# Optimization experiments

Measured on AMD Instinct MI355X. Metric: run time of the kernel, lower is better.

## Reference

```python
import jax, jax.numpy as jnp
import numpy as np

D_MODEL = 1024
N_HEADS = 16
HEAD_DIM = D_MODEL // N_HEADS
B, T = 2, 2048

def setup_inputs() -> dict:
    key = jax.random.key(0)
    ks = jax.random.split(key, 9)
    s = 1.0 / np.sqrt(D_MODEL)
    return {
        "x": jax.random.normal(ks[0], (B, T, D_MODEL), dtype=jnp.float32),
        "Wq": jax.random.normal(ks[1], (D_MODEL, D_MODEL), dtype=jnp.float32) * s,
        "bq": jax.random.normal(ks[2], (D_MODEL,), dtype=jnp.float32) * 0.01,
        "Wk": jax.random.normal(ks[3], (D_MODEL, D_MODEL), dtype=jnp.float32) * s,
        "bk": jax.random.normal(ks[4], (D_MODEL,), dtype=jnp.float32) * 0.01,
        "Wv": jax.random.normal(ks[5], (D_MODEL, D_MODEL), dtype=jnp.float32) * s,
        "bv": jax.random.normal(ks[6], (D_MODEL,), dtype=jnp.float32) * 0.01,
        "Wo": jax.random.normal(ks[7], (D_MODEL, D_MODEL), dtype=jnp.float32) * s,
        "bo": jax.random.normal(ks[8], (D_MODEL,), dtype=jnp.float32) * 0.01,
    }

def reference(x, Wq, bq, Wk, bk, Wv, bv, Wo, bo):
    b, t, c = x.shape
    # Projections; reshape to [B, H, T, Dh]
    def heads(w, bias):
        return (x @ w.T + bias).reshape(b, t, N_HEADS, HEAD_DIM).transpose(0, 2, 1, 3)
    q = heads(Wq, bq)
    k = heads(Wk, bk)
    v = heads(Wv, bv)
    scale = 1.0 / np.sqrt(HEAD_DIM)
    att = jnp.einsum("bhqd,bhkd->bhqk", q, k) * scale  # [B,H,T,T]
    causal = jnp.tril(jnp.ones((t, t), dtype=bool))
    att = jnp.where(causal, att, -jnp.inf)
    att = jax.nn.softmax(att, axis=-1)
    # dropout p=0.0 (eval) -> identity
    y = jnp.einsum("bhqk,bhkd->bhqd", att, v)  # [B,H,T,Dh]
    y = y.transpose(0, 2, 1, 3).reshape(b, t, c)
    return y @ Wo.T + bo
```

## Files before the change

### kernel.cpp

```cpp
#include <hip/hip_runtime.h>
#include <stdint.h>


typedef unsigned short u16;
typedef __attribute__((ext_vector_type(8)))  __bf16 bf16x8;
typedef __attribute__((ext_vector_type(4)))  float  f32x4;
typedef __attribute__((ext_vector_type(16))) float  f32x16;
typedef __attribute__((ext_vector_type(4)))  float  float4v;
typedef __attribute__((ext_vector_type(4)))  unsigned short u16x4;
typedef __attribute__((ext_vector_type(4)))  unsigned int   u32x4;
typedef __attribute__((ext_vector_type(8)))  short  short8;

#define BB 2
#define TT 2048
#define DD 1024
#define HH 16
#define DH 64
#define MM (BB*TT)
#define NSLOT 2304
#define CEXP 0.18033688011f

static __device__ __forceinline__ u16 f2bf(float f) {
    uint32_t u = __builtin_bit_cast(uint32_t, f);
    u += 0x7FFFu + ((u >> 16) & 1u);
    return (u16)(u >> 16);
}
static __device__ __forceinline__ float bf2f(u16 v) {
    uint32_t u = (uint32_t)v << 16;
    return __builtin_bit_cast(float, u);
}

static __device__ __forceinline__ unsigned cvt_pk_bf16(float a, float b) {
    unsigned r;
    asm("v_cvt_pk_bf16_f32 %0, %1, %2" : "=v"(r) : "v"(a), "v"(b));
    return r;
}

static __device__ __forceinline__ void load_lds16(const u16* g, const u16* lds_base) {
    __builtin_amdgcn_global_load_lds(
        (const __attribute__((address_space(1))) void*)(uintptr_t)g,
        (__attribute__((address_space(3)))  void*)(uint32_t)(uintptr_t)lds_base,
        16u, 0, 0u);
}

static __device__ __forceinline__ f32x4 mfma16(bf16x8 a, bf16x8 b, f32x4 c) {
    return __builtin_amdgcn_mfma_f32_16x16x32_bf16(a, b, c, 0, 0, 0);
}
static __device__ __forceinline__ f32x16 mfma32(bf16x8 a, bf16x8 b, f32x16 c) {
    return __builtin_amdgcn_mfma_f32_32x32x16_bf16(a, b, c, 0, 0, 0);
}

static __device__ __forceinline__ float tree_sum16(const f32x16& a) {
    float m[8];
#pragma unroll
    for (int r = 0; r < 8; ++r) m[r] = a[r] + a[r + 8];
#pragma unroll
    for (int off = 4; off; off >>= 1)
#pragma unroll
        for (int r = 0; r < off; ++r) m[r] += m[r + off];
    return m[0];
}

static __device__ __forceinline__ bf16x8 pack8(float s0, float s1, float s2,
        float s3, float s4, float s5, float s6, float s7) {
    unsigned c0 = cvt_pk_bf16(s0, s1);
    unsigned c1 = cvt_pk_bf16(s2, s3);
    unsigned c2 = cvt_pk_bf16(s4, s5);
    unsigned c3 = cvt_pk_bf16(s6, s7);
    asm volatile("v_permlane32_swap_b32 %0, %1" : "+v"(c0), "+v"(c2));
    asm volatile("v_permlane32_swap_b32 %0, %1" : "+v"(c1), "+v"(c3));
    u32x4 w; w[0] = c0; w[1] = c1; w[2] = c2; w[3] = c3;
    return __builtin_bit_cast(bf16x8, w);
}

__global__ __launch_bounds__(256) void cvt_kernel(const float* __restrict__ src,
                                                  u16* __restrict__ dst, int n4) {
    int i = blockIdx.x * blockDim.x + threadIdx.x;
    int stride = gridDim.x * blockDim.x;
    for (; i < n4; i += stride) {
        float4v v = ((const float4v*)src)[i];
        u16x4 o;
        o[0] = f2bf(v[0]); o[1] = f2bf(v[1]); o[2] = f2bf(v[2]); o[3] = f2bf(v[3]);
        ((u16x4*)dst)[i] = o;
    }
}

__global__ __launch_bounds__(256) void cvt4_kernel(const float* __restrict__ s0,
        const float* __restrict__ s1, const float* __restrict__ s2,
        const float* __restrict__ s3, u16* __restrict__ d0, u16* __restrict__ d1,
        u16* __restrict__ d2, u16* __restrict__ d3, int n4) {
    const int z = blockIdx.y;
    const float* src = (z == 0) ? s0 : (z == 1) ? s1 : (z == 2) ? s2 : s3;
    u16* dst = (z == 0) ? d0 : (z == 1) ? d1 : (z == 2) ? d2 : d3;
    const float sc = (z == 0) ? CEXP : 1.0f;
    int i = blockIdx.x * blockDim.x + threadIdx.x;
    int stride = gridDim.x * blockDim.x;
    for (; i < n4; i += stride) {
        float4v v = ((const float4v*)src)[i];
        u16x4 o;
        o[0] = f2bf(v[0] * sc); o[1] = f2bf(v[1] * sc);
        o[2] = f2bf(v[2] * sc); o[3] = f2bf(v[3] * sc);
        ((u16x4*)dst)[i] = o;
    }
}

template<int OUTF32>
__global__ __launch_bounds__(256) void gemm_nt(const u16* __restrict__ A,
        const u16* __restrict__ W,
        const float* __restrict__ b0, const float* __restrict__ b1,
        const float* __restrict__ b2, float qsc,
        u16* __restrict__ outb, float* __restrict__ outf,
        int M, int N, int K) {
    __shared__ alignas(16) u16 As[128 * 32];
    __shared__ alignas(16) u16 Bs[128 * 32];

    const int tid  = threadIdx.x;
    const int wave = tid >> 6, lane = tid & 63;
    const int lr = lane & 15, lg = lane >> 4;
    const int wr = wave >> 1, wc = wave & 1;
    const int z  = blockIdx.z;
    const int m0 = blockIdx.x * 128;
    const int n0 = blockIdx.y * 128;

    const u16* Wz = W + (size_t)z * N * K;
    const float* bias = (z == 0) ? b0 : (z == 1) ? b1 : b2;
    const float bsc = (z == 0) ? qsc : 1.0f;

    f32x4 acc[4][4];
#pragma unroll
    for (int m = 0; m < 4; ++m)
#pragma unroll
        for (int n = 0; n < 4; ++n) acc[m][n] = (f32x4){0.f, 0.f, 0.f, 0.f};

    for (int k0 = 0; k0 < K; k0 += 32) {
        __syncthreads();
#pragma unroll
        for (int it = 0; it < 2; ++it) {
            int c = it * 256 + tid;
            int row = c >> 2, cc = (c & 3) * 8;
            const u16* gA = A  + (size_t)(m0 + row) * K + k0 + cc;
            const u16* gB = Wz + (size_t)(n0 + row) * K + k0 + cc;
            load_lds16(gA, As + (size_t)(it * 256 + wave * 64) * 8);
            load_lds16(gB, Bs + (size_t)(it * 256 + wave * 64) * 8);
        }
        __syncthreads();

        bf16x8 af[4], bfm[4];
#pragma unroll
        for (int m = 0; m < 4; ++m)
            af[m] = *(const bf16x8*)&As[(wr * 64 + m * 16 + lr) * 32 + lg * 8];
#pragma unroll
        for (int n = 0; n < 4; ++n)
            bfm[n] = *(const bf16x8*)&Bs[(wc * 64 + n * 16 + lr) * 32 + lg * 8];
#pragma unroll
        for (int m = 0; m < 4; ++m)
#pragma unroll
            for (int n = 0; n < 4; ++n)
                acc[m][n] = mfma16(af[m], bfm[n], acc[m][n]);
    }

#pragma unroll
    for (int n = 0; n < 4; ++n) {
        int col = n0 + wc * 64 + n * 16 + lr;
        float bv = bias[col] * bsc;
#pragma unroll
        for (int m = 0; m < 4; ++m) {
            int row = m0 + wr * 64 + m * 16 + lg * 4;
            if (OUTF32 == 0 && z == 2) {
                u16* vt = outb + (size_t)2 * M * N;
                size_t base = ((size_t)(((row >> 11) * 16 + (col >> 6)) * 64
                                        + (col & 63))) * 2048 + (row & 2047);
                u16x4 pv;
#pragma unroll
                for (int r = 0; r < 4; ++r) pv[r] = f2bf(acc[m][n][r] + bv);
                *(u16x4*)&vt[base] = pv;
            } else {
#pragma unroll
                for (int r = 0; r < 4; ++r) {
                    float v = acc[m][n][r] + bv;
                    if (OUTF32 == 0)
                        outb[(size_t)z * M * N + (size_t)(row + r) * N + col] = f2bf(v);
                    else
                        outf[(size_t)(row + r) * N + col] = v;
                }
            }
        }
    }
}

__global__ __launch_bounds__(256) void attn_part(const u16* __restrict__ Qb,
        const u16* __restrict__ Kb, const u16* __restrict__ VTb,
        u16* __restrict__ Op, float* __restrict__ Ml, u16* __restrict__ Yb) {
    __shared__ alignas(16) u16 Ks[64 * 64];
    __shared__ alignas(16) u16 Vs[64 * 64];

    const int tid  = threadIdx.x;
    const int wave = tid >> 6, lane = tid & 63;
    const int lq = lane & 31, hi = lane >> 5;

    const int i0 = blockIdx.x;
    const int bh = (i0 & 7) * 4 + ((i0 >> 3) / 72);
    const int s  = (i0 >> 3) % 72;
    int qi = 0, ch = 0;
    {
        int cum = 0, found = 0;
#pragma unroll
        for (int j = 0; j < 16; ++j) {
            int n = (j + 2) >> 1;
            if (!found && s < cum + n) { qi = j; ch = s - cum; found = 1; }
            cum += n;
        }
    }
    const int nc = (qi + 2) >> 1;
    const int b = bh >> 4, h = bh & 15;
    const size_t rb = (size_t)b * TT;
    const int hoff = h * DH;
    const int q0w = qi * 128 + wave * 32;
    const int k0 = ch * 256;
    const int kend = qi * 128 + 128;
    const int k1 = (k0 + 256 < kend) ? k0 + 256 : kend;

    const int srow0 = tid >> 3, sl = tid & 7;
    const int srow1 = (256 + tid) >> 3;

    const u16* Kbh = Kb + rb * DD + hoff;
    const u16* Vbh = VTb + (size_t)bh * 64 * 2048;

    bf16x8 qf[4];
    {
        const u16* qrow = Qb + (rb + q0w + lq) * DD + hoff + hi * 8;
#pragma unroll
        for (int kc = 0; kc < 4; ++kc) qf[kc] = *(const bf16x8*)(qrow + kc * 16);
    }

    f32x16 o0 = {}, o1 = {};
    float l_i = 0.f;

    for (int kv0 = k0; kv0 < k1; kv0 += 64) {
        __syncthreads();
        load_lds16(Kbh + (size_t)(kv0 + srow0) * DD + (sl ^ (srow0 & 7)) * 8,
                   &Ks[(size_t)(wave * 64) * 8]);
        load_lds16(Kbh + (size_t)(kv0 + srow1) * DD + (sl ^ (srow1 & 7)) * 8,
                   &Ks[(size_t)(256 + wave * 64) * 8]);
        load_lds16(Vbh + (size_t)srow0 * 2048 + kv0 + (sl ^ (srow0 & 7)) * 8,
                   &Vs[(size_t)(wave * 64) * 8]);
        load_lds16(Vbh + (size_t)srow1 * 2048 + kv0 + (sl ^ (srow1 & 7)) * 8,
                   &Vs[(size_t)(256 + wave * 64) * 8]);
        __syncthreads();

        if (kv0 < q0w + 32) {
            const int rowm = lq & 7;
            const bool diag = (kv0 + 63 > q0w);
            const int qrel = q0w + lq - kv0;
            bf16x8 pb[4];

            {
                f32x16 st = {};
#pragma unroll
                for (int kc = 0; kc < 4; ++kc) {
                    bf16x8 kf = *(const bf16x8*)&Ks[lq * 64 + ((2 * kc + hi) ^ rowm) * 8];
                    st = mfma32(kf, qf[kc], st);
                }
                if (diag) {
#pragma unroll
                    for (int r = 0; r < 16; ++r) {
                        int key = (r & 3) + 8 * (r >> 2) + 4 * hi;
                        if (key > qrel) st[r] = -1e30f;
                    }
                }
#pragma unroll
                for (int r = 0; r < 16; ++r) st[r] = __builtin_amdgcn_exp2f(st[r]);
                l_i += tree_sum16(st);
                pb[0] = pack8(st[0], st[1], st[2], st[3], st[4], st[5], st[6], st[7]);
                pb[1] = pack8(st[8], st[9], st[10], st[11], st[12], st[13], st[14], st[15]);
            }
            {
                f32x16 st = {};
#pragma unroll
                for (int kc = 0; kc < 4; ++kc) {
                    bf16x8 kf = *(const bf16x8*)&Ks[(32 + lq) * 64 + ((2 * kc + hi) ^ rowm) * 8];
                    st = mfma32(kf, qf[kc], st);
                }
                if (diag) {
#pragma unroll
                    for (int r = 0; r < 16; ++r) {
                        int key = 32 + (r & 3) + 8 * (r >> 2) + 4 * hi;
                        if (key > qrel) st[r] = -1e30f;
                    }
                }
#pragma unroll
                for (int r = 0; r < 16; ++r) st[r] = __builtin_amdgcn_exp2f(st[r]);
                l_i += tree_sum16(st);
                pb[2] = pack8(st[0], st[1], st[2], st[3], st[4], st[5], st[6], st[7]);
                pb[3] = pack8(st[8], st[9], st[10], st[11], st[12], st[13], st[14], st[15]);
            }

#pragma unroll
            for (int ks = 0; ks < 4; ++ks) {
                bf16x8 vf0 = *(const bf16x8*)&Vs[lq * 64        + ((ks * 2 + hi) ^ rowm) * 8];
                bf16x8 vf1 = *(const bf16x8*)&Vs[(32 + lq) * 64 + ((ks * 2 + hi) ^ rowm) * 8];
                o0 = mfma32(vf0, pb[ks], o0);
                o1 = mfma32(vf1, pb[ks], o1);
            }
        }
    }

    l_i += __shfl_xor(l_i, 32);
    const int col = wave * 32 + lq;

    if (nc == 1) {
        const float inv = 1.0f / l_i;
        u16* yrow = Yb + (rb + q0w + lq) * DD + hoff;
#pragma unroll
        for (int g = 0; g < 4; ++g) {
            u16x4 p0, p1;
#pragma unroll
            for (int j = 0; j < 4; ++j) {
                p0[j] = f2bf(o0[4 * g + j] * inv);
                p1[j] = f2bf(o1[4 * g + j] * inv);
            }
            *(u16x4*)&yrow[8 * g + 4 * hi]      = p0;
            *(u16x4*)&yrow[32 + 8 * g + 4 * hi] = p1;
        }
    } else {
        const int slot = bh * 72 + s;
        u16* op = Op + (size_t)slot * 8192;
#pragma unroll
        for (int r = 0; r < 16; ++r) {
            const int d0 = (r & 3) + 8 * (r >> 2) + 4 * hi;
            op[d0 * 128 + col]        = f2bf(o0[r]);
            op[(32 + d0) * 128 + col] = f2bf(o1[r]);
        }
        if (hi == 0) Ml[(size_t)slot * 128 + col] = l_i;
    }
}

__global__ __launch_bounds__(256) void attn_merge(const u16* __restrict__ Op,
        const float* __restrict__ Ml, u16* __restrict__ Yb) {
    const int bq = blockIdx.x;
    const int bh = bq >> 4, qi = bq & 15;
    const int nc = (qi + 2) >> 1;
    if (nc == 1) return;
    int cum = 0;
#pragma unroll
    for (int j = 0; j < 16; ++j) cum += (j < qi) ? ((j + 2) >> 1) : 0;
    const int s0 = bh * 72 + cum;

    const int t = threadIdx.x;
    const int row = t >> 1, dh = (t & 1) * 32;

    float L = 0.f;
    float acc[32];
#pragma unroll
    for (int d = 0; d < 32; ++d) acc[d] = 0.f;
#pragma unroll
    for (int c = 0; c < 8; ++c) {
        if (c < nc) {
            L += Ml[(size_t)(s0 + c) * 128 + row];
            const u16* op = Op + (size_t)(s0 + c) * 8192 + row;
#pragma unroll
            for (int d = 0; d < 32; ++d)
                acc[d] += bf2f(op[(dh + d) * 128]);
        }
    }
    const float inv = 1.0f / L;

    const int b = bh >> 4, h = bh & 15;
    u16* yrow = Yb + ((size_t)(b * TT + qi * 128 + row)) * DD + h * DH + dh;
#pragma unroll
    for (int g = 0; g < 8; ++g) {
        u16x4 p;
#pragma unroll
        for (int j = 0; j < 4; ++j) p[j] = f2bf(acc[4 * g + j] * inv);
        *(u16x4*)&yrow[4 * g] = p;
    }
}

extern "C" void kernel_launch(void* const* d_in, const int* in_sizes, int n_in,
                              void* d_out, int out_size, void* d_ws, size_t ws_size,
                              hipStream_t stream) {
    const float* x  = (const float*)d_in[0];
    const float* Wq = (const float*)d_in[1];
    const float* bq = (const float*)d_in[2];
    const float* Wk = (const float*)d_in[3];
    const float* bk = (const float*)d_in[4];
    const float* Wv = (const float*)d_in[5];
    const float* bv = (const float*)d_in[6];
    const float* Wo = (const float*)d_in[7];
    const float* bo = (const float*)d_in[8];
    float* out = (float*)d_out;

    const size_t XN = (size_t)MM * DD;
    const size_t WN = (size_t)DD * DD;

    u16* xb  = (u16*)d_ws;
    u16* Wb  = xb  + XN;
    u16* Wob = Wb  + 3 * WN;
    u16* QKV = Wob + WN;
    u16* Yb  = QKV + 3 * XN;
    u16* Op  = Yb  + XN;
    float* Ml = (float*)(Op + (size_t)NSLOT * 8192);

    cvt_kernel<<<2048, 256, 0, stream>>>(x, xb, (int)(XN / 4));
    cvt4_kernel<<<dim3(256, 4), 256, 0, stream>>>(Wq, Wk, Wv, Wo,
            Wb, Wb + WN, Wb + 2 * WN, Wob, (int)(WN / 4));

    gemm_nt<0><<<dim3(32, 8, 3), 256, 0, stream>>>(xb, Wb, bq, bk, bv, CEXP,
                                                   QKV, nullptr, MM, DD, DD);
    attn_part<<<NSLOT, 256, 0, stream>>>(QKV, QKV + XN, QKV + 2 * XN,
                                         Op, Ml, Yb);
    attn_merge<<<512, 256, 0, stream>>>(Op, Ml, Yb);
    gemm_nt<1><<<dim3(32, 8, 1), 256, 0, stream>>>(Yb, Wob, bo, bo, bo, 1.0f,
                                                   nullptr, out, MM, DD, DD);
}
```

Baseline: 132.4 us.

## Double-buffer GEMM and attention LDS, compute V transposed, coarsen KV chunks

```diff
diff --git a/kernel.cpp b/kernel.cpp
--- a/kernel.cpp
+++ b/kernel.cpp
@@ -17,8 +17,10 @@
 #define HH 16
 #define DH 64
 #define MM (BB*TT)
-#define NSLOT 2304
+#define NSLOT 1280
 #define CEXP 0.18033688011f
+#define XNE ((size_t)MM*DD)
+#define WNE ((size_t)DD*DD)
 
 static __device__ __forceinline__ u16 f2bf(float f) {
     uint32_t u = __builtin_bit_cast(uint32_t, f);
@@ -104,27 +106,40 @@
     }
 }
 
-template<int OUTF32>
-__global__ __launch_bounds__(256) void gemm_nt(const u16* __restrict__ A,
-        const u16* __restrict__ W,
-        const float* __restrict__ b0, const float* __restrict__ b1,
-        const float* __restrict__ b2, float qsc,
-        u16* __restrict__ outb, float* __restrict__ outf,
-        int M, int N, int K) {
-    __shared__ alignas(16) u16 As[128 * 32];
-    __shared__ alignas(16) u16 Bs[128 * 32];
+template<int MODE>
+__global__ __launch_bounds__(256) void gemm2(const u16* __restrict__ xb,
+        const u16* __restrict__ Wb, const float* __restrict__ bq,
+        const float* __restrict__ bk, const float* __restrict__ bvv,
+        u16* __restrict__ outq, u16* __restrict__ vt, float* __restrict__ outf) {
+    __shared__ alignas(16) u16 As[2][128 * 32];
+    __shared__ alignas(16) u16 Bs[2][128 * 32];
 
     const int tid  = threadIdx.x;
     const int wave = tid >> 6, lane = tid & 63;
     const int lr = lane & 15, lg = lane >> 4;
     const int wr = wave >> 1, wc = wave & 1;
-    const int z  = blockIdx.z;
-    const int m0 = blockIdx.x * 128;
-    const int n0 = blockIdx.y * 128;
-
-    const u16* Wz = W + (size_t)z * N * K;
-    const float* bias = (z == 0) ? b0 : (z == 1) ? b1 : b2;
-    const float bsc = (z == 0) ? qsc : 1.0f;
+    const int K = 1024;
+
+    const u16 *Ap, *Wp;
+    int m0, n0, zb = 0;
+    bool vtmode = false;
+    const int id = blockIdx.x;
+    if (MODE == 0) {
+        if (id < 512) {
+            zb = id >> 8; int r = id & 255;
+            m0 = (r >> 3) * 128; n0 = (r & 7) * 128;
+            Ap = xb; Wp = Wb + (size_t)zb * WNE;
+        } else {
+            int v = id - 512; zb = v >> 7; int r = v & 127;
+            m0 = (r >> 4) * 128; n0 = (r & 15) * 128;
+            Ap = Wb + 2 * WNE;
+            Wp = xb + (size_t)zb * 2048 * 1024;
+            vtmode = true;
+        }
+    } else {
+        m0 = (id >> 3) * 128; n0 = (id & 7) * 128;
+        Ap = xb; Wp = Wb;
+    }
 
     f32x4 acc[4][4];
 #pragma unroll
@@ -132,57 +147,86 @@
 #pragma unroll
         for (int n = 0; n < 4; ++n) acc[m][n] = (f32x4){0.f, 0.f, 0.f, 0.f};
 
+#define G_STAGE(BB_, KK_)                                                     \
+    {                                                                         \
+        _Pragma("unroll")                                                     \
+        for (int it = 0; it < 2; ++it) {                                      \
+            int c = it * 256 + tid;                                           \
+            int row = c >> 2, cc = (c & 3) * 8;                               \
+            load_lds16(Ap + (size_t)(m0 + row) * K + (KK_) + cc,              \
+                       &As[BB_][(size_t)(it * 256 + wave * 64) * 8]);         \
+            load_lds16(Wp + (size_t)(n0 + row) * K + (KK_) + cc,              \
+                       &Bs[BB_][(size_t)(it * 256 + wave * 64) * 8]);         \
+        }                                                                     \
+    }
+
+    G_STAGE(0, 0);
+    __syncthreads();
+    int cur = 0;
     for (int k0 = 0; k0 < K; k0 += 32) {
-        __syncthreads();
-#pragma unroll
-        for (int it = 0; it < 2; ++it) {
-            int c = it * 256 + tid;
-            int row = c >> 2, cc = (c & 3) * 8;
-            const u16* gA = A  + (size_t)(m0 + row) * K + k0 + cc;
-            const u16* gB = Wz + (size_t)(n0 + row) * K + k0 + cc;
-            load_lds16(gA, As + (size_t)(it * 256 + wave * 64) * 8);
-            load_lds16(gB, Bs + (size_t)(it * 256 + wave * 64) * 8);
-        }
-        __syncthreads();
+        if (k0 + 32 < K) G_STAGE(cur ^ 1, k0 + 32);
 
         bf16x8 af[4], bfm[4];
 #pragma unroll
         for (int m = 0; m < 4; ++m)
-            af[m] = *(const bf16x8*)&As[(wr * 64 + m * 16 + lr) * 32 + lg * 8];
+            af[m] = *(const bf16x8*)&As[cur][(wr * 64 + m * 16 + lr) * 32 + lg * 8];
 #pragma unroll
         for (int n = 0; n < 4; ++n)
-            bfm[n] = *(const bf16x8*)&Bs[(wc * 64 + n * 16 + lr) * 32 + lg * 8];
+            bfm[n] = *(const bf16x8*)&Bs[cur][(wc * 64 + n * 16 + lr) * 32 + lg * 8];
 #pragma unroll
         for (int m = 0; m < 4; ++m)
 #pragma unroll
             for (int n = 0; n < 4; ++n)
                 acc[m][n] = mfma16(af[m], bfm[n], acc[m][n]);
-    }
-
-#pragma unroll
-    for (int n = 0; n < 4; ++n) {
-        int col = n0 + wc * 64 + n * 16 + lr;
-        float bv = bias[col] * bsc;
+
+        __syncthreads();
+        cur ^= 1;
+    }
+#undef G_STAGE
+
+    if (MODE == 1) {
+#pragma unroll
+        for (int n = 0; n < 4; ++n) {
+            int col = n0 + wc * 64 + n * 16 + lr;
+            float bvl = bq[col];
+#pragma unroll
+            for (int m = 0; m < 4; ++m) {
+                int row = m0 + wr * 64 + m * 16 + lg * 4;
+#pragma unroll
+                for (int r = 0; r < 4; ++r)
+                    outf[(size_t)(row + r) * 1024 + col] = acc[m][n][r] + bvl;
+            }
+        }
+    } else if (!vtmode) {
+        const float* bias = zb ? bk : bq;
+        const float bsc = zb ? 1.0f : CEXP;
+#pragma unroll
+        for (int n = 0; n < 4; ++n) {
+            int col = n0 + wc * 64 + n * 16 + lr;
+            float bvl = bias[col] * bsc;
+#pragma unroll
+            for (int m = 0; m < 4; ++m) {
+                int row = m0 + wr * 64 + m * 16 + lg * 4;
+#pragma unroll
+                for (int r = 0; r < 4; ++r)
+                    outq[(size_t)zb * XNE + (size_t)(row + r) * 1024 + col] =
+                        f2bf(acc[m][n][r] + bvl);
+            }
+        }
+    } else {
+        u16* vo = vt + (size_t)zb * 1024 * 2048;
 #pragma unroll
         for (int m = 0; m < 4; ++m) {
-            int row = m0 + wr * 64 + m * 16 + lg * 4;
-            if (OUTF32 == 0 && z == 2) {
-                u16* vt = outb + (size_t)2 * M * N;
-                size_t base = ((size_t)(((row >> 11) * 16 + (col >> 6)) * 64
-                                        + (col & 63))) * 2048 + (row & 2047);
-                u16x4 pv;
-#pragma unroll
-                for (int r = 0; r < 4; ++r) pv[r] = f2bf(acc[m][n][r] + bv);
-                *(u16x4*)&vt[base] = pv;
-            } else {
-#pragma unroll
-                for (int r = 0; r < 4; ++r) {
-                    float v = acc[m][n][r] + bv;
-                    if (OUTF32 == 0)
-                        outb[(size_t)z * M * N + (size_t)(row + r) * N + col] = f2bf(v);
-                    else
-                        outf[(size_t)(row + r) * N + col] = v;
-                }
+            int rowb = m0 + wr * 64 + m * 16 + lg * 4;
+            float bvr[4];
+#pragma unroll
+            for (int r = 0; r < 4; ++r) bvr[r] = bvv[rowb + r];
+#pragma unroll
+            for (int n = 0; n < 4; ++n) {
+                int col = n0 + wc * 64 + n * 16 + lr;
+#pragma unroll
+                for (int r = 0; r < 4; ++r)
+                    vo[(size_t)(rowb + r) * 2048 + col] = f2bf(acc[m][n][r] + bvr[r]);
             }
         }
     }
@@ -191,34 +235,34 @@
 __global__ __launch_bounds__(256) void attn_part(const u16* __restrict__ Qb,
         const u16* __restrict__ Kb, const u16* __restrict__ VTb,
         u16* __restrict__ Op, float* __restrict__ Ml, u16* __restrict__ Yb) {
-    __shared__ alignas(16) u16 Ks[64 * 64];
-    __shared__ alignas(16) u16 Vs[64 * 64];
+    __shared__ alignas(16) u16 Ks[2][64 * 64];
+    __shared__ alignas(16) u16 Vs[2][64 * 64];
 
     const int tid  = threadIdx.x;
     const int wave = tid >> 6, lane = tid & 63;
     const int lq = lane & 31, hi = lane >> 5;
 
     const int i0 = blockIdx.x;
-    const int bh = (i0 & 7) * 4 + ((i0 >> 3) / 72);
-    const int s  = (i0 >> 3) % 72;
+    const int bh = (i0 & 7) * 4 + ((i0 >> 3) / 40);
+    const int s  = (i0 >> 3) % 40;
     int qi = 0, ch = 0;
     {
         int cum = 0, found = 0;
 #pragma unroll
         for (int j = 0; j < 16; ++j) {
-            int n = (j + 2) >> 1;
+            int n = (j >> 2) + 1;
             if (!found && s < cum + n) { qi = j; ch = s - cum; found = 1; }
             cum += n;
         }
     }
-    const int nc = (qi + 2) >> 1;
+    const int nc = (qi >> 2) + 1;
     const int b = bh >> 4, h = bh & 15;
     const size_t rb = (size_t)b * TT;
     const int hoff = h * DH;
     const int q0w = qi * 128 + wave * 32;
-    const int k0 = ch * 256;
+    const int k0 = ch * 512;
     const int kend = qi * 128 + 128;
-    const int k1 = (k0 + 256 < kend) ? k0 + 256 : kend;
+    const int k1 = (k0 + 512 < kend) ? k0 + 512 : kend;
 
     const int srow0 = tid >> 3, sl = tid & 7;
     const int srow1 = (256 + tid) >> 3;
@@ -236,17 +280,24 @@
     f32x16 o0 = {}, o1 = {};
     float l_i = 0.f;
 
+#define A_STAGE(BB_, KV_)                                                     \
+    {                                                                         \
+        load_lds16(Kbh + (size_t)((KV_) + srow0) * DD + (sl ^ (srow0 & 7)) * 8,\
+                   &Ks[BB_][(size_t)(wave * 64) * 8]);                        \
+        load_lds16(Kbh + (size_t)((KV_) + srow1) * DD + (sl ^ (srow1 & 7)) * 8,\
+                   &Ks[BB_][(size_t)(256 + wave * 64) * 8]);                  \
+        load_lds16(Vbh + (size_t)srow0 * 2048 + (KV_) + (sl ^ (srow0 & 7)) * 8,\
+                   &Vs[BB_][(size_t)(wave * 64) * 8]);                        \
+        load_lds16(Vbh + (size_t)srow1 * 2048 + (KV_) + (sl ^ (srow1 & 7)) * 8,\
+                   &Vs[BB_][(size_t)(256 + wave * 64) * 8]);                  \
+    }
+
+    A_STAGE(0, k0);
+    __syncthreads();
+    int cur = 0;
+
     for (int kv0 = k0; kv0 < k1; kv0 += 64) {
-        __syncthreads();
-        load_lds16(Kbh + (size_t)(kv0 + srow0) * DD + (sl ^ (srow0 & 7)) * 8,
-                   &Ks[(size_t)(wave * 64) * 8]);
-        load_lds16(Kbh + (size_t)(kv0 + srow1) * DD + (sl ^ (srow1 & 7)) * 8,
-                   &Ks[(size_t)(256 + wave * 64) * 8]);
-        load_lds16(Vbh + (size_t)srow0 * 2048 + kv0 + (sl ^ (srow0 & 7)) * 8,
-                   &Vs[(size_t)(wave * 64) * 8]);
-        load_lds16(Vbh + (size_t)srow1 * 2048 + kv0 + (sl ^ (srow1 & 7)) * 8,
-                   &Vs[(size_t)(256 + wave * 64) * 8]);
-        __syncthreads();
+        if (kv0 + 64 < k1) A_STAGE(cur ^ 1, kv0 + 64);
 
         if (kv0 < q0w + 32) {
             const int rowm = lq & 7;
@@ -256,11 +307,13 @@
 
             {
                 f32x16 st = {};
+                __builtin_amdgcn_s_setprio(1);
 #pragma unroll
                 for (int kc = 0; kc < 4; ++kc) {
-                    bf16x8 kf = *(const bf16x8*)&Ks[lq * 64 + ((2 * kc + hi) ^ rowm) * 8];
+                    bf16x8 kf = *(const bf16x8*)&Ks[cur][lq * 64 + ((2 * kc + hi) ^ rowm) * 8];
                     st = mfma32(kf, qf[kc], st);
                 }
+                __builtin_amdgcn_s_setprio(0);
                 if (diag) {
 #pragma unroll
                     for (int r = 0; r < 16; ++r) {
@@ -276,11 +329,13 @@
             }
             {
                 f32x16 st = {};
+                __builtin_amdgcn_s_setprio(1);
 #pragma unroll
                 for (int kc = 0; kc < 4; ++kc) {
-                    bf16x8 kf = *(const bf16x8*)&Ks[(32 + lq) * 64 + ((2 * kc + hi) ^ rowm) * 8];
+                    bf16x8 kf = *(const bf16x8*)&Ks[cur][(32 + lq) * 64 + ((2 * kc + hi) ^ rowm) * 8];
                     st = mfma32(kf, qf[kc], st);
                 }
+                __builtin_amdgcn_s_setprio(0);
                 if (diag) {
 #pragma unroll
                     for (int r = 0; r < 16; ++r) {
@@ -295,15 +350,21 @@
                 pb[3] = pack8(st[8], st[9], st[10], st[11], st[12], st[13], st[14], st[15]);
             }
 
+            __builtin_amdgcn_s_setprio(1);
 #pragma unroll
             for (int ks = 0; ks < 4; ++ks) {
-                bf16x8 vf0 = *(const bf16x8*)&Vs[lq * 64        + ((ks * 2 + hi) ^ rowm) * 8];
-                bf16x8 vf1 = *(const bf16x8*)&Vs[(32 + lq) * 64 + ((ks * 2 + hi) ^ rowm) * 8];
+                bf16x8 vf0 = *(const bf16x8*)&Vs[cur][lq * 64        + ((ks * 2 + hi) ^ rowm) * 8];
+                bf16x8 vf1 = *(const bf16x8*)&Vs[cur][(32 + lq) * 64 + ((ks * 2 + hi) ^ rowm) * 8];
                 o0 = mfma32(vf0, pb[ks], o0);
                 o1 = mfma32(vf1, pb[ks], o1);
             }
-        }
-    }
+            __builtin_amdgcn_s_setprio(0);
+        }
+
+        __syncthreads();
+        cur ^= 1;
+    }
+#undef A_STAGE
 
     l_i += __shfl_xor(l_i, 32);
     const int col = wave * 32 + lq;
@@ -323,7 +384,7 @@
             *(u16x4*)&yrow[32 + 8 * g + 4 * hi] = p1;
         }
     } else {
-        const int slot = bh * 72 + s;
+        const int slot = bh * 40 + s;
         u16* op = Op + (size_t)slot * 8192;
 #pragma unroll
         for (int r = 0; r < 16; ++r) {
@@ -339,12 +400,12 @@
         const float* __restrict__ Ml, u16* __restrict__ Yb) {
     const int bq = blockIdx.x;
     const int bh = bq >> 4, qi = bq & 15;
-    const int nc = (qi + 2) >> 1;
+    const int nc = (qi >> 2) + 1;
     if (nc == 1) return;
     int cum = 0;
 #pragma unroll
-    for (int j = 0; j < 16; ++j) cum += (j < qi) ? ((j + 2) >> 1) : 0;
-    const int s0 = bh * 72 + cum;
+    for (int j = 0; j < 16; ++j) cum += (j < qi) ? ((j >> 2) + 1) : 0;
+    const int s0 = bh * 40 + cum;
 
     const int t = threadIdx.x;
     const int row = t >> 1, dh = (t & 1) * 32;
@@ -354,7 +415,7 @@
 #pragma unroll
     for (int d = 0; d < 32; ++d) acc[d] = 0.f;
 #pragma unroll
-    for (int c = 0; c < 8; ++c) {
+    for (int c = 0; c < 4; ++c) {
         if (c < nc) {
             L += Ml[(size_t)(s0 + c) * 128 + row];
             const u16* op = Op + (size_t)(s0 + c) * 8192 + row;
@@ -390,26 +451,23 @@
     const float* bo = (const float*)d_in[8];
     float* out = (float*)d_out;
 
-    const size_t XN = (size_t)MM * DD;
-    const size_t WN = (size_t)DD * DD;
-
     u16* xb  = (u16*)d_ws;
-    u16* Wb  = xb  + XN;
-    u16* Wob = Wb  + 3 * WN;
-    u16* QKV = Wob + WN;
-    u16* Yb  = QKV + 3 * XN;
-    u16* Op  = Yb  + XN;
+    u16* Wb  = xb  + XNE;
+    u16* Wob = Wb  + 3 * WNE;
+    u16* QKV = Wob + WNE;
+    u16* Yb  = QKV + 3 * XNE;
+    u16* Op  = Yb  + XNE;
     float* Ml = (float*)(Op + (size_t)NSLOT * 8192);
 
-    cvt_kernel<<<2048, 256, 0, stream>>>(x, xb, (int)(XN / 4));
+    cvt_kernel<<<2048, 256, 0, stream>>>(x, xb, (int)(XNE / 4));
     cvt4_kernel<<<dim3(256, 4), 256, 0, stream>>>(Wq, Wk, Wv, Wo,
-            Wb, Wb + WN, Wb + 2 * WN, Wob, (int)(WN / 4));
-
-    gemm_nt<0><<<dim3(32, 8, 3), 256, 0, stream>>>(xb, Wb, bq, bk, bv, CEXP,
-                                                   QKV, nullptr, MM, DD, DD);
-    attn_part<<<NSLOT, 256, 0, stream>>>(QKV, QKV + XN, QKV + 2 * XN,
+            Wb, Wb + WNE, Wb + 2 * WNE, Wob, (int)(WNE / 4));
+
+    gemm2<0><<<768, 256, 0, stream>>>(xb, Wb, bq, bk, bv,
+                                      QKV, QKV + 2 * XNE, nullptr);
+    attn_part<<<NSLOT, 256, 0, stream>>>(QKV, QKV + XNE, QKV + 2 * XNE,
                                          Op, Ml, Yb);
     attn_merge<<<512, 256, 0, stream>>>(Op, Ml, Yb);
-    gemm_nt<1><<<dim3(32, 8, 1), 256, 0, stream>>>(Yb, Wob, bo, bo, bo, 1.0f,
-                                                   nullptr, out, MM, DD, DD);
-}
+    gemm2<1><<<256, 256, 0, stream>>>(Yb, Wob, bo, nullptr, nullptr,
+                                      nullptr, nullptr, out);
+}
```

Result: faster. 120.3 us (-9.2%).
